# Optimization experiments

Measured on AMD Instinct MI355X. Metric: run time of the kernel, lower is better.

Reference implementation:

```python
import jax, jax.numpy as jnp
import numpy as np

B, T, C, M = 64, 1024, 256, 1024  # note: broadcast in the torch source forces M == T


def setup_inputs() -> dict:
    key = jax.random.key(0)
    k = jax.random.split(key, 6)
    x = jax.random.normal(k[0], (B, T, C), jnp.float32)
    memory = 0.02 * jax.random.normal(k[1], (1, M, C), jnp.float32)  # nn.init.normal_(std=0.02)
    w1 = jax.random.normal(k[2], (2 * C, 4 * C), jnp.float32) / np.sqrt(2 * C)
    b1 = jnp.zeros((4 * C,), jnp.float32)
    w2 = jax.random.normal(k[3], (4 * C, C), jnp.float32) / np.sqrt(4 * C)
    b2 = jnp.zeros((C,), jnp.float32)
    return {"x": x, "memory": memory, "w1": w1, "b1": b1, "w2": w2, "b2": b2}


def reference(x, memory, w1, b1, w2, b2):
    # x: [B,T,C], memory: [1,M,C] (shared across batch, expanded lazily)
    mem = memory[0]                                        # [M,C]
    energy = jnp.einsum('btc,mc->btm', x, mem)             # cross-attn scores
    weights = jax.nn.softmax(energy, axis=-1)              # [B,T,M]
    retrieved = jnp.einsum('btm,mc->btc', weights, mem)    # [B,T,C]
    cat = jnp.concatenate([x, retrieved], axis=-1)         # [B,T,2C] (forward output)
    # gate MLP: Linear(2C,4C) -> SiLU -> Linear(4C,C) -> Sigmoid
    h = jax.nn.silu(jnp.einsum('btk,kf->btf', cat, w1) + b1)
    update_gate = jax.nn.sigmoid(jnp.einsum('btf,fc->btc', h, w2) + b2)  # [B,T,C], T==M
    # memory blend + batch-mean reduction (side-effect update in torch, detached)
    x_mean = jnp.mean(x, axis=1, keepdims=True)            # [B,1,C]
    new_mem = memory * (1.0 - update_gate) + x_mean * update_gate  # [B,M,C]
    new_memory = jnp.mean(new_mem, axis=0, keepdims=True)  # [1,M,C]
    return cat, new_memory
```

## Files before the change

### kernel.cpp

```cpp
#include <hip/hip_runtime.h>
#include <hip/hip_bf16.h>


#define BT 65536

typedef short bf16x8 __attribute__((ext_vector_type(8)));
typedef float f32x4 __attribute__((ext_vector_type(4)));

__device__ __forceinline__ unsigned short f2bf(float f) {
    unsigned x = __float_as_uint(f);
    unsigned r = (x + 0x7FFFu + ((x >> 16) & 1u)) >> 16;
    return (unsigned short)r;
}
__device__ __forceinline__ float bf2f(unsigned short u) {
    return __uint_as_float(((unsigned)u) << 16);
}

__device__ __forceinline__ void async16(const unsigned short* g, unsigned short* l) {
    __builtin_amdgcn_global_load_lds((const __attribute__((address_space(1))) unsigned int*)g,
                                     (__attribute__((address_space(3))) unsigned int*)l,
                                     16, 0, 0);
}


__global__ __launch_bounds__(256) void prep_x(const float* __restrict__ x,
                                              float* __restrict__ cat_out,
                                              unsigned short* __restrict__ cat_b) {
    long tid = (long)blockIdx.x * 256 + threadIdx.x;
    long i4 = tid * 4;
    long row = i4 >> 8;
    int c = (int)(i4 & 255);
    float4 v = *(const float4*)&x[i4];
    *(float4*)&cat_out[row * 512 + c] = v;
    ushort4 b4;
    b4.x = f2bf(v.x); b4.y = f2bf(v.y); b4.z = f2bf(v.z); b4.w = f2bf(v.w);
    *(ushort4*)&cat_b[row * 512 + c] = b4;
}

__global__ __launch_bounds__(256) void prep_mem(const float* __restrict__ mem,
                                                unsigned short* __restrict__ mem_b,
                                                unsigned short* __restrict__ memT_b) {
    int tid = blockIdx.x * 256 + threadIdx.x;
    mem_b[tid] = f2bf(mem[tid]);
    int c = tid >> 10, m = tid & 1023;
    memT_b[tid] = f2bf(mem[m * 256 + c]);
}

__global__ __launch_bounds__(256) void prep_w1(const float* __restrict__ w1,
                                               unsigned short* __restrict__ w1T) {
    int tid = blockIdx.x * 256 + threadIdx.x;
    int f = tid >> 9, k = tid & 511;
    w1T[tid] = f2bf(w1[k * 1024 + f]);
}

__global__ __launch_bounds__(256) void prep_w2(const float* __restrict__ w2,
                                               unsigned short* __restrict__ w2T) {
    int tid = blockIdx.x * 256 + threadIdx.x;
    int c = tid >> 10, k = tid & 1023;
    w2T[tid] = f2bf(w2[k * 256 + c]);
}

__global__ __launch_bounds__(256) void xmean_k(const float* __restrict__ x,
                                               float* __restrict__ xmean) {
    int b = blockIdx.x;
    int t0 = blockIdx.y * 64;
    int c = threadIdx.x;
    float s = 0.f;
    for (int t = 0; t < 64; t++)
        s += x[((long)(b * 1024 + t0 + t)) * 256 + c];
    atomicAdd(&xmean[b * 256 + c], s * (1.f / 1024.f));
}


__device__ __forceinline__ void compute_tile(const unsigned short* bufA,
                                             const unsigned short* bufB,
                                             const int* aoff, const int* boff,
                                             f32x4 acc[4][4]) {
    bf16x8 af[4], bfr[4];
#pragma unroll
    for (int i = 0; i < 4; i++) af[i] = *(const bf16x8*)&bufA[aoff[i]];
#pragma unroll
    for (int j = 0; j < 4; j++) bfr[j] = *(const bf16x8*)&bufB[boff[j]];
#pragma unroll
    for (int i = 0; i < 4; i++)
#pragma unroll
        for (int j = 0; j < 4; j++)
            acc[i][j] = __builtin_amdgcn_mfma_f32_16x16x32_bf16(af[i], bfr[j], acc[i][j], 0, 0, 0);
}

template <int MODE>
__global__ __launch_bounds__(256) void gemm_bt(const unsigned short* __restrict__ A, long lda,
                                               const unsigned short* __restrict__ Bt, int K,
                                               float* __restrict__ outF,
                                               unsigned short* __restrict__ outB,
                                               const float* __restrict__ bias) {
    const int t = threadIdx.x;
    const int wave = t >> 6, lane = t & 63;
    const int waveM = wave >> 1, waveN = wave & 1;
    const int quad = lane >> 4, l16 = lane & 15;

    const int nwg = gridDim.x * gridDim.y;
    const int lid = blockIdx.y * gridDim.x + blockIdx.x;
    const int sid = (lid & 7) * (nwg >> 3) + (lid >> 3);
    const int nb = sid % gridDim.x;
    const int mb = sid / gridDim.x;
    const long n0 = (long)nb * 128;
    const long m0 = (long)mb * 128;

    __shared__ unsigned short lA[2][128 * 32];
    __shared__ unsigned short lB[2][128 * 32];

    f32x4 acc[4][4] = {};

    const int sRow = wave * 16 + (lane >> 2);
    const int sC = (lane & 3) ^ ((sRow >> 1) & 3);
    const unsigned short* Ag0 = A + (m0 + sRow) * lda + sC * 8;
    const unsigned short* Ag1 = Ag0 + 64 * lda;
    const unsigned short* Bg0 = Bt + (n0 + sRow) * (long)K + sC * 8;
    const unsigned short* Bg1 = Bg0 + 64 * (long)K;
    const int so0 = wave * 512;
    const int so1 = 2048 + wave * 512;

    const int sx = (l16 >> 1) & 3;
    int aoff[4], boff[4];
#pragma unroll
    for (int i = 0; i < 4; i++) {
        aoff[i] = (waveM * 64 + i * 16 + l16) * 32 + ((quad ^ sx) * 8);
        boff[i] = (waveN * 64 + i * 16 + l16) * 32 + ((quad ^ sx) * 8);
    }

#define STAGE(BUF, KOFF) do {                       \
        async16(Ag0 + (KOFF), &lA[BUF][so0]);       \
        async16(Ag1 + (KOFF), &lA[BUF][so1]);       \
        async16(Bg0 + (KOFF), &lB[BUF][so0]);       \
        async16(Bg1 + (KOFF), &lB[BUF][so1]);       \
    } while (0)

#define WAITBAR() do {                                      \
        asm volatile("s_waitcnt vmcnt(0)" ::: "memory");    \
        __builtin_amdgcn_s_barrier();                       \
        __builtin_amdgcn_sched_barrier(0);                  \
    } while (0)

    const int nk = K >> 5;
    STAGE(0, 0);
    WAITBAR();

    int cur = 0;
    for (int kt = 0; kt < nk - 1; ++kt) {
        STAGE(cur ^ 1, (kt + 1) << 5);
        compute_tile(&lA[cur][0], &lB[cur][0], aoff, boff, acc);
        WAITBAR();
        cur ^= 1;
    }
    compute_tile(&lA[cur][0], &lB[cur][0], aoff, boff, acc);

#undef STAGE
#undef WAITBAR

#pragma unroll
    for (int i = 0; i < 4; i++) {
#pragma unroll
        for (int j = 0; j < 4; j++) {
            long col = n0 + waveN * 64 + j * 16 + l16;
            float bval = (MODE == 2 || MODE == 3) ? bias[col] : 0.f;
#pragma unroll
            for (int r = 0; r < 4; r++) {
                long row = m0 + waveM * 64 + i * 16 + quad * 4 + r;
                float v = acc[i][j][r];
                if (MODE == 0) {
                    outB[row * 1024 + col] = f2bf(v);
                } else if (MODE == 1) {
                    long o = row * 512 + 256 + col;
                    outF[o] = v;
                    outB[o] = f2bf(v);
                } else if (MODE == 2) {
                    float z = v + bval;
                    float s = 1.f / (1.f + __expf(-z));
                    outB[row * 1024 + col] = f2bf(z * s);
                } else {
                    float z = v + bval;
                    outF[row * 256 + col] = 1.f / (1.f + __expf(-z));
                }
            }
        }
    }
}

__global__ __launch_bounds__(256) void softmax_rows(unsigned short* __restrict__ P) {
    long row = (long)blockIdx.x * 4 + (threadIdx.x >> 6);
    int lane = threadIdx.x & 63;
    unsigned short* p = P + row * 1024 + lane * 16;
    uint4 u0 = *(const uint4*)p;
    uint4 u1 = *(const uint4*)(p + 8);
    const unsigned short* ua = (const unsigned short*)&u0;
    const unsigned short* ub = (const unsigned short*)&u1;
    float v[16];
#pragma unroll
    for (int i = 0; i < 8; i++) { v[i] = bf2f(ua[i]); v[i + 8] = bf2f(ub[i]); }
    float m = -1e30f;
#pragma unroll
    for (int i = 0; i < 16; i++) m = fmaxf(m, v[i]);
    for (int off = 32; off >= 1; off >>= 1) m = fmaxf(m, __shfl_xor(m, off));
    float s = 0.f;
#pragma unroll
    for (int i = 0; i < 16; i++) { v[i] = __expf(v[i] - m); s += v[i]; }
    for (int off = 32; off >= 1; off >>= 1) s += __shfl_xor(s, off);
    float inv = 1.f / s;
    unsigned short o[16];
#pragma unroll
    for (int i = 0; i < 16; i++) o[i] = f2bf(v[i] * inv);
    *(uint4*)p = *(uint4*)&o[0];
    *(uint4*)(p + 8) = *(uint4*)&o[8];
}

__global__ __launch_bounds__(256) void reduce_mem(const float* __restrict__ gate,
                                                  const float* __restrict__ memory,
                                                  const float* __restrict__ xmean,
                                                  float* __restrict__ out2) {
    int m = blockIdx.x, c = threadIdx.x;
    float mm = memory[m * 256 + c];
    float s = 0.f;
    for (int b = 0; b < 64; b++)
        s += gate[((long)(b * 1024 + m)) * 256 + c] * (xmean[b * 256 + c] - mm);
    out2[m * 256 + c] = mm + s * (1.f / 64.f);
}

extern "C" void kernel_launch(void* const* d_in, const int* in_sizes, int n_in,
                              void* d_out, int out_size, void* d_ws, size_t ws_size,
                              hipStream_t stream) {
    const float* x      = (const float*)d_in[0];
    const float* memory = (const float*)d_in[1];
    const float* w1     = (const float*)d_in[2];
    const float* b1     = (const float*)d_in[3];
    const float* w2     = (const float*)d_in[4];
    const float* b2     = (const float*)d_in[5];
    float* out = (float*)d_out;

    unsigned short* mem_b  = (unsigned short*)d_ws;
    unsigned short* memT_b = mem_b + 262144;
    unsigned short* w1T    = memT_b + 262144;
    unsigned short* w2T    = w1T + 524288;
    float* xmean           = (float*)(w2T + 262144);
    unsigned short* cat_b  = (unsigned short*)(xmean + 16384);
    unsigned short* Pbuf   = cat_b + 33554432;
    float* gate            = (float*)cat_b;

    hipMemsetAsync(xmean, 0, 64 * 256 * sizeof(float), stream);

    prep_mem<<<1024, 256, 0, stream>>>(memory, mem_b, memT_b);
    prep_w1<<<2048, 256, 0, stream>>>(w1, w1T);
    prep_w2<<<1024, 256, 0, stream>>>(w2, w2T);
    prep_x<<<16384, 256, 0, stream>>>(x, out, cat_b);
    xmean_k<<<dim3(64, 16), 256, 0, stream>>>(x, xmean);

    gemm_bt<0><<<dim3(8, 512), 256, 0, stream>>>(cat_b, 512, mem_b, 256, nullptr, Pbuf, nullptr);
    softmax_rows<<<16384, 256, 0, stream>>>(Pbuf);
    gemm_bt<1><<<dim3(2, 512), 256, 0, stream>>>(Pbuf, 1024, memT_b, 1024, out, cat_b, nullptr);
    gemm_bt<2><<<dim3(8, 512), 256, 0, stream>>>(cat_b, 512, w1T, 512, nullptr, Pbuf, b1);
    gemm_bt<3><<<dim3(2, 512), 256, 0, stream>>>(Pbuf, 1024, w2T, 1024, gate, nullptr, b2);

    reduce_mem<<<1024, 256, 0, stream>>>(gate, memory, xmean, out + 33554432);
}
```

Before: 579.2 us.

## Triple-buffer GEMM LDS staging with partial vmcnt waits and compile-time K

Result: faster. 550.9 us (-4.9%).

```diff
diff --git a/kernel.cpp b/kernel.cpp
--- a/kernel.cpp
+++ b/kernel.cpp
@@ -88,12 +88,14 @@
             acc[i][j] = __builtin_amdgcn_mfma_f32_16x16x32_bf16(af[i], bfr[j], acc[i][j], 0, 0, 0);
 }
 
-template <int MODE>
-__global__ __launch_bounds__(256) void gemm_bt(const unsigned short* __restrict__ A, long lda,
-                                               const unsigned short* __restrict__ Bt, int K,
+template <int MODE, int K>
+__global__ __launch_bounds__(256) void gemm_bt(const unsigned short* __restrict__ A,
+                                               const unsigned short* __restrict__ Bt,
                                                float* __restrict__ outF,
                                                unsigned short* __restrict__ outB,
                                                const float* __restrict__ bias) {
+    constexpr long LDA = (MODE == 0 || MODE == 2) ? 512 : 1024;
+    constexpr int NK = K / 32;
     const int t = threadIdx.x;
     const int wave = t >> 6, lane = t & 63;
     const int waveM = wave >> 1, waveN = wave & 1;
@@ -107,15 +109,15 @@
     const long n0 = (long)nb * 128;
     const long m0 = (long)mb * 128;
 
-    __shared__ unsigned short lA[2][128 * 32];
-    __shared__ unsigned short lB[2][128 * 32];
+    __shared__ unsigned short lA[3][128 * 32];
+    __shared__ unsigned short lB[3][128 * 32];
 
     f32x4 acc[4][4] = {};
 
     const int sRow = wave * 16 + (lane >> 2);
     const int sC = (lane & 3) ^ ((sRow >> 1) & 3);
-    const unsigned short* Ag0 = A + (m0 + sRow) * lda + sC * 8;
-    const unsigned short* Ag1 = Ag0 + 64 * lda;
+    const unsigned short* Ag0 = A + (m0 + sRow) * LDA + sC * 8;
+    const unsigned short* Ag1 = Ag0 + 64 * LDA;
     const unsigned short* Bg0 = Bt + (n0 + sRow) * (long)K + sC * 8;
     const unsigned short* Bg1 = Bg0 + 64 * (long)K;
     const int so0 = wave * 512;
@@ -129,34 +131,37 @@
         boff[i] = (waveN * 64 + i * 16 + l16) * 32 + ((quad ^ sx) * 8);
     }
 
-#define STAGE(BUF, KOFF) do {                       \
-        async16(Ag0 + (KOFF), &lA[BUF][so0]);       \
-        async16(Ag1 + (KOFF), &lA[BUF][so1]);       \
-        async16(Bg0 + (KOFF), &lB[BUF][so0]);       \
-        async16(Bg1 + (KOFF), &lB[BUF][so1]);       \
+#define STAGE(BUF, KT) do {                                   \
+        async16(Ag0 + (KT) * 32, &lA[BUF][so0]);              \
+        async16(Ag1 + (KT) * 32, &lA[BUF][so1]);              \
+        async16(Bg0 + (KT) * 32, &lB[BUF][so0]);              \
+        async16(Bg1 + (KT) * 32, &lB[BUF][so1]);              \
     } while (0)
 
-#define WAITBAR() do {                                      \
-        asm volatile("s_waitcnt vmcnt(0)" ::: "memory");    \
-        __builtin_amdgcn_s_barrier();                       \
-        __builtin_amdgcn_sched_barrier(0);                  \
-    } while (0)
-
-    const int nk = K >> 5;
     STAGE(0, 0);
-    WAITBAR();
-
-    int cur = 0;
-    for (int kt = 0; kt < nk - 1; ++kt) {
-        STAGE(cur ^ 1, (kt + 1) << 5);
-        compute_tile(&lA[cur][0], &lB[cur][0], aoff, boff, acc);
-        WAITBAR();
-        cur ^= 1;
+    STAGE(1, 1);
+    asm volatile("s_waitcnt vmcnt(4)" ::: "memory");
+    __builtin_amdgcn_s_barrier();
+    __builtin_amdgcn_sched_barrier(0);
+
+#pragma unroll
+    for (int kt = 0; kt < NK; ++kt) {
+        if (kt + 2 < NK) {
+            STAGE((kt + 2) % 3, kt + 2);
+            __builtin_amdgcn_sched_barrier(0);
+        }
+        compute_tile(&lA[kt % 3][0], &lB[kt % 3][0], aoff, boff, acc);
+        if (kt + 2 < NK) {
+            asm volatile("s_waitcnt vmcnt(4) lgkmcnt(0)" ::: "memory");
+            __builtin_amdgcn_s_barrier();
+            __builtin_amdgcn_sched_barrier(0);
+        } else if (kt + 1 < NK) {
+            asm volatile("s_waitcnt vmcnt(0) lgkmcnt(0)" ::: "memory");
+            __builtin_amdgcn_s_barrier();
+            __builtin_amdgcn_sched_barrier(0);
+        }
     }
-    compute_tile(&lA[cur][0], &lB[cur][0], aoff, boff, acc);
-
 #undef STAGE
-#undef WAITBAR
 
 #pragma unroll
     for (int i = 0; i < 4; i++) {
@@ -254,11 +259,11 @@
     prep_x<<<16384, 256, 0, stream>>>(x, out, cat_b);
     xmean_k<<<dim3(64, 16), 256, 0, stream>>>(x, xmean);
 
-    gemm_bt<0><<<dim3(8, 512), 256, 0, stream>>>(cat_b, 512, mem_b, 256, nullptr, Pbuf, nullptr);
+    gemm_bt<0, 256><<<dim3(8, 512), 256, 0, stream>>>(cat_b, mem_b, nullptr, Pbuf, nullptr);
     softmax_rows<<<16384, 256, 0, stream>>>(Pbuf);
-    gemm_bt<1><<<dim3(2, 512), 256, 0, stream>>>(Pbuf, 1024, memT_b, 1024, out, cat_b, nullptr);
-    gemm_bt<2><<<dim3(8, 512), 256, 0, stream>>>(cat_b, 512, w1T, 512, nullptr, Pbuf, b1);
-    gemm_bt<3><<<dim3(2, 512), 256, 0, stream>>>(Pbuf, 1024, w2T, 1024, gate, nullptr, b2);
+    gemm_bt<1, 1024><<<dim3(2, 512), 256, 0, stream>>>(Pbuf, memT_b, out, cat_b, nullptr);
+    gemm_bt<2, 512><<<dim3(8, 512), 256, 0, stream>>>(cat_b, w1T, nullptr, Pbuf, b1);
+    gemm_bt<3, 1024><<<dim3(2, 512), 256, 0, stream>>>(Pbuf, w2T, gate, nullptr, b2);
 
     reduce_mem<<<1024, 256, 0, stream>>>(gate, memory, xmean, out + 33554432);
 }
```
